# Performance work log

Measured on AMD Instinct MI355X. Metric: run time of the kernel, lower is better.

The kernel has to match this reference:

```python
import jax, jax.numpy as jnp
import numpy as np

EPS = 1e-5

def _fake_quant(w, axis):
    # symmetric int8 fake-quant with straight-through estimator
    s = jnp.max(jnp.abs(w), axis=axis, keepdims=True) / 127.0 + 1e-8
    q = jnp.clip(jnp.round(w / s), -127.0, 127.0) * s
    return w + jax.lax.stop_gradient(q - w)

def _qconv1x1(x, w, b):
    # x: [B, C_in, Q, H, W]; w: [C_out, C_in] (1x1 kernel); weight fake-quantized
    wq = _fake_quant(w, axis=1)
    return jnp.einsum('bcqhw,oc->boqhw', x, wq) + b[None, :, None, None, None]

def setup_inputs() -> dict:
    key = jax.random.key(0)
    ks = jax.random.split(key, 12)
    B, C, Q, H, W = 8, 256, 4, 40, 40
    x = jax.random.normal(ks[0], (B, C, Q, H, W), dtype=jnp.float32)
    scale = 1.0 / np.sqrt(C)
    Wq = jax.random.normal(ks[1], (C, C), dtype=jnp.float32) * scale
    Wk = jax.random.normal(ks[2], (C, C), dtype=jnp.float32) * scale
    Wv = jax.random.normal(ks[3], (C, C), dtype=jnp.float32) * scale
    Wp = jax.random.normal(ks[4], (C, C), dtype=jnp.float32) * scale
    bq = jnp.zeros((C,), jnp.float32)
    bk = jnp.zeros((C,), jnp.float32)
    bv = jnp.zeros((C,), jnp.float32)
    bp = jnp.zeros((C,), jnp.float32)
    gamma = jnp.ones((C,), jnp.float32)
    beta = jnp.zeros((C,), jnp.float32)
    return {"x": x, "Wq": Wq, "bq": bq, "Wk": Wk, "bk": bk,
            "Wv": Wv, "bv": bv, "Wp": Wp, "bp": bp,
            "gamma": gamma, "beta": beta}

def reference(x, Wq, bq, Wk, bk, Wv, bv, Wp, bp, gamma, beta):
    B, C, Q, H, W = x.shape
    q = _qconv1x1(x, Wq, bq)
    k = _qconv1x1(x, Wk, bk)
    v = _qconv1x1(x, Wv, bv)
    # per-rotation channel attention: [B, Q=4, C, H*W]
    qh = q.reshape(B, C, Q, H * W).transpose(0, 2, 1, 3)
    kh = k.reshape(B, C, Q, H * W).transpose(0, 2, 1, 3)
    vh = v.reshape(B, C, Q, H * W).transpose(0, 2, 1, 3)
    scale = 1.0 / jnp.sqrt(jnp.float32(C // 4))
    attn = jnp.einsum('bqcn,bqdn->bqcd', qh, kh) * scale  # [B,4,C,C]
    attn = jax.nn.softmax(attn, axis=-1)
    out = jnp.einsum('bqcd,bqdn->bqcn', attn, vh)  # [B,4,C,HW]
    out = out.transpose(0, 2, 1, 3).reshape(B, C, Q, H, W)
    out = _qconv1x1(out, Wp, bp)
    # IQBN: per-channel batchnorm with int8 fake-quantized gamma
    mean = jnp.mean(out, axis=(0, 2, 3, 4), keepdims=True)
    var = jnp.var(out, axis=(0, 2, 3, 4), keepdims=True)
    g = _fake_quant(gamma, axis=None)[None, :, None, None, None]
    b = beta[None, :, None, None, None]
    out = (out - mean) * jax.lax.rsqrt(var + EPS) * g + b
    return out
```

## Files before the change

### kernel.cpp

```cpp
#include <hip/hip_runtime.h>
#include <math.h>

#define BB 8
#define CCH 256
#define QQ 4
#define NN 1600
#define BQN 32
#define SP 51200
#define EPSF 1e-5f

typedef __attribute__((ext_vector_type(8))) short bf16x8;
typedef __attribute__((ext_vector_type(4))) float f32x4;

static __device__ inline ushort f2bf(float f) {
  union { float f; unsigned u; } v; v.f = f;
  return (ushort)((v.u + 0x7fffu + ((v.u >> 16) & 1u)) >> 16);
}
static __device__ inline float bf2f(ushort u) {
  union { unsigned u; float f; } v; v.u = ((unsigned)u) << 16;
  return v.f;
}
static __device__ inline void gld16(const ushort* g, ushort* l) {
  __builtin_amdgcn_global_load_lds(
      (const __attribute__((address_space(1))) unsigned int*)g,
      (__attribute__((address_space(3))) unsigned int*)l, 16, 0, 0);
}

__global__ __launch_bounds__(256)
void qp_kernel(const float* __restrict__ Wq, const float* __restrict__ Wk,
               const float* __restrict__ Wv, const float* __restrict__ Wp,
               const float* __restrict__ gamma, const float* __restrict__ x,
               ushort* __restrict__ wq, ushort* __restrict__ wk,
               ushort* __restrict__ wvT, ushort* __restrict__ wp,
               ushort* __restrict__ wqT, ushort* __restrict__ wkT,
               ushort* __restrict__ wpT, float* __restrict__ gq,
               ushort* __restrict__ xb, ushort* __restrict__ xT,
               float* __restrict__ rpart) {
  __shared__ float red[256];
  __shared__ ushort lT[64 * 66];
  int blk = blockIdx.x;
  int tid = threadIdx.x;
  if (blk < 1024) {
    int mat = blk >> 8;
    int row = blk & 255;
    const float* W = (mat == 0) ? Wq : (mat == 1) ? Wk : (mat == 2) ? Wv : Wp;
    float w = W[row * 256 + tid];
    red[tid] = fabsf(w);
    __syncthreads();
    for (int s = 128; s > 0; s >>= 1) {
      if (tid < s) red[tid] = fmaxf(red[tid], red[tid + s]);
      __syncthreads();
    }
    float s = red[0] / 127.0f + 1e-8f;
    float q = fminf(fmaxf(rintf(w / s), -127.0f), 127.0f) * s;
    ushort qb = f2bf(q);
    if (mat == 0)      { wq[row * 256 + tid] = qb; wqT[tid * 256 + row] = qb; }
    else if (mat == 1) { wk[row * 256 + tid] = qb; wkT[tid * 256 + row] = qb; }
    else if (mat == 2) { wvT[tid * 256 + row] = qb; }
    else               { wp[row * 256 + tid] = qb; wpT[tid * 256 + row] = qb; }
    return;
  }
  if (blk == 1024) {
    float g = gamma[tid];
    red[tid] = fabsf(g);
    __syncthreads();
    for (int s = 128; s > 0; s >>= 1) {
      if (tid < s) red[tid] = fmaxf(red[tid], red[tid + s]);
      __syncthreads();
    }
    float s = red[0] / 127.0f + 1e-8f;
    gq[tid] = fminf(fmaxf(rintf(g / s), -127.0f), 127.0f) * s;
    return;
  }
  int p = blk - 1025;
  int sx = p % 25;
  int rem = p / 25;
  int cy = rem & 3, bqi = rem >> 2;
  int b = bqi >> 2, q = bqi & 3;
  int s0 = sx * 64, c0 = cy * 64;
  int c = tid >> 2, nch = (tid & 3) * 16;
  const float* xp = x + ((size_t)(b * CCH + c0 + c) * QQ + q) * NN + s0 + nch;
  union { ushort u[16]; int4 v[2]; } nb;
  float s = 0.f;
#pragma unroll
  for (int j = 0; j < 4; j++) {
    float4 f = ((const float4*)xp)[j];
    ushort b0 = f2bf(f.x), b1 = f2bf(f.y), b2 = f2bf(f.z), b3 = f2bf(f.w);
    s += bf2f(b0) + bf2f(b1) + bf2f(b2) + bf2f(b3);
    nb.u[j * 4 + 0] = b0;
    nb.u[j * 4 + 1] = b1;
    nb.u[j * 4 + 2] = b2;
    nb.u[j * 4 + 3] = b3;
    lT[c * 66 + nch + j * 4 + 0] = b0;
    lT[c * 66 + nch + j * 4 + 1] = b1;
    lT[c * 66 + nch + j * 4 + 2] = b2;
    lT[c * 66 + nch + j * 4 + 3] = b3;
  }
  ushort* xbp = xb + (size_t)bqi * (CCH * NN) + (size_t)(c0 + c) * NN + s0 + nch;
  *(int4*)xbp = nb.v[0];
  *((int4*)xbp + 1) = nb.v[1];
  s += __shfl_down(s, 2);
  s += __shfl_down(s, 1);
  if ((tid & 3) == 0) rpart[((size_t)bqi * 25 + sx) * 256 + c0 + c] = s;
  __syncthreads();
  int n = tid >> 2, cch = (tid & 3) * 16;
  union { ushort u[16]; int4 v[2]; } o;
#pragma unroll
  for (int i = 0; i < 16; i++) o.u[i] = lT[(cch + i) * 66 + n];
  ushort* dst = xT + (size_t)(bqi * NN + s0 + n) * CCH + c0 + cch;
  *(int4*)dst = o.v[0];
  *((int4*)dst + 1) = o.v[1];
}

__global__ __launch_bounds__(256)
void gram_uv_kernel(const ushort* __restrict__ xb, ushort* __restrict__ Gh,
                    ushort* __restrict__ Gl,
                    const ushort* __restrict__ wqT, const ushort* __restrict__ wkT,
                    const float* __restrict__ rpart, float* __restrict__ r,
                    float* __restrict__ u, float* __restrict__ vv) {
  __shared__ __align__(16) char smem[16384];
  __shared__ float rs[256];
  int lin = blockIdx.x + 11 * blockIdx.y;
  int k8 = lin & 7, j = lin >> 3;
  int z = 4 * k8 + j / 11, t = j % 11;
  int tid = threadIdx.x;
  if (t == 10) {
    float rv = 0.f;
#pragma unroll
    for (int k = 0; k < 25; k++) rv += rpart[((size_t)z * 25 + k) * 256 + tid];
    rs[tid] = rv;
    r[z * 256 + tid] = rv;
    __syncthreads();
    float su = 0.f, sv = 0.f;
    for (int i = 0; i < 256; i++) {
      float rr = rs[i];
      su += bf2f(wqT[i * 256 + tid]) * rr;
      sv += bf2f(wkT[i * 256 + tid]) * rr;
    }
    u[z * 256 + tid] = su;
    vv[z * 256 + tid] = sv;
    return;
  }
  int ty = (t >= 4) + (t >= 7) + (t >= 9);
  int base = ty * 4 - (ty * (ty - 1)) / 2;
  int tx = ty + (t - base);
  int mBase = ty * 64, nBase = tx * 64;
  bool offd = (tx != ty);
  int wave = tid >> 6, lane = tid & 63;
  int wm = wave >> 1, wn = wave & 1;
  int col = lane & 15, quad = lane >> 4;
  const ushort* X = xb + (size_t)z * (CCH * NN);
  const ushort* gA = X + (size_t)(mBase + (tid >> 2)) * NN + (tid & 3) * 8;
  const ushort* gB = X + (size_t)(nBase + (tid >> 2)) * NN + (tid & 3) * 8;
  f32x4 acc[2][2];
#pragma unroll
  for (int i = 0; i < 2; i++)
#pragma unroll
    for (int j2 = 0; j2 < 2; j2++) acc[i][j2] = (f32x4){0.f, 0.f, 0.f, 0.f};

  const int nIter = NN / 32;
  gld16(gA, (ushort*)smem + tid * 8);
  gld16(gB, (ushort*)(smem + 4096) + tid * 8);
  for (int it = 0; it < nIter; ++it) {
    int cur = it & 1;
    __syncthreads();
    if (it + 1 < nIter) {
      int kt = (it + 1) << 5;
      char* bb = smem + (cur ^ 1) * 8192;
      gld16(gA + kt, (ushort*)bb + tid * 8);
      gld16(gB + kt, (ushort*)(bb + 4096) + tid * 8);
    }
    const ushort* lA = (const ushort*)(smem + cur * 8192);
    const ushort* lB = lA + 2048;
    bf16x8 af[2], bfr[2];
#pragma unroll
    for (int i = 0; i < 2; i++)
      af[i] = *(const bf16x8*)&lA[(wm * 32 + i * 16 + col) * 32 + quad * 8];
#pragma unroll
    for (int j2 = 0; j2 < 2; j2++)
      bfr[j2] = *(const bf16x8*)&lB[(wn * 32 + j2 * 16 + col) * 32 + quad * 8];
#pragma unroll
    for (int i = 0; i < 2; i++)
#pragma unroll
      for (int j2 = 0; j2 < 2; j2++)
        acc[i][j2] = __builtin_amdgcn_mfma_f32_16x16x32_bf16(af[i], bfr[j2], acc[i][j2], 0, 0, 0);
  }
  __syncthreads();
  float* lCw = (float*)smem + wave * 576;
#pragma unroll
  for (int i = 0; i < 2; i++) {
#pragma unroll
    for (int j2 = 0; j2 < 2; j2++)
#pragma unroll
      for (int rg = 0; rg < 4; rg++)
        lCw[(quad * 4 + rg) * 36 + j2 * 16 + col] = acc[i][j2][rg];
    int mrow0 = mBase + wm * 32 + i * 16;
    int nW = nBase + wn * 32;
    int rr = lane >> 2, cc = (lane & 3) * 8;
    union { ushort u[8]; int4 v; } oh, ol;
#pragma unroll
    for (int t8 = 0; t8 < 8; t8++) {
      float vfl = lCw[rr * 36 + cc + t8];
      ushort hh = f2bf(vfl);
      oh.u[t8] = hh;
      ol.u[t8] = f2bf(vfl - bf2f(hh));
    }
    size_t off = (size_t)z * 65536 + (size_t)(mrow0 + rr) * 256 + nW + cc;
    *(int4*)(Gh + off) = oh.v;
    *(int4*)(Gl + off) = ol.v;
    if (offd) {
      int nn = lane >> 1, mh = (lane & 1) * 8;
      union { ushort u[8]; int4 v; } th, tl;
#pragma unroll
      for (int t8 = 0; t8 < 8; t8++) {
        float vfl = lCw[(mh + t8) * 36 + nn];
        ushort hh = f2bf(vfl);
        th.u[t8] = hh;
        tl.u[t8] = f2bf(vfl - bf2f(hh));
      }
      size_t offT = (size_t)z * 65536 + (size_t)(nW + nn) * 256 + mrow0 + mh;
      *(int4*)(Gh + offT) = th.v;
      *(int4*)(Gl + offT) = tl.v;
    }
  }
}

__global__ __launch_bounds__(256)
void spk_kernel(const ushort* __restrict__ wq, const ushort* __restrict__ Gh,
                const ushort* __restrict__ Gl, const ushort* __restrict__ wk,
                const float* __restrict__ ug, const float* __restrict__ vg,
                const float* __restrict__ bqv, const float* __restrict__ bkv,
                const float* __restrict__ bvv,
                ushort* __restrict__ P, float* __restrict__ pb) {
  __shared__ __align__(16) char smem[103424];
  int lin = blockIdx.x + 8 * blockIdx.y;
  int k8 = lin & 7, j9 = lin >> 3;
  int z = 4 * k8 + (j9 >> 3), mBase = (j9 & 7) * 32;
  int tid = threadIdx.x, wave = tid >> 6, lane = tid & 63;
  int col = lane & 15, quad = lane >> 4;
  int rA = tid >> 2, sub = (tid & 3) * 8;
  const ushort* Ghz = Gh + (size_t)z * 65536;
  const ushort* Glz = Gl + (size_t)z * 65536;
  ushort* M1h_l = (ushort*)(smem + 69632);
  ushort* M1l_l = M1h_l + 8448;

  f32x4 acc[2][4];
#pragma unroll
  for (int i = 0; i < 2; i++)
#pragma unroll
    for (int j = 0; j < 4; j++) acc[i][j] = (f32x4){0.f, 0.f, 0.f, 0.f};

  auto s1_load = [&](int buf, int kt) {
    ushort* L = (ushort*)(smem + buf * 34816);
    if (tid < 128)
      gld16(wq + (size_t)(mBase + rA) * 256 + kt + sub, L + tid * 8);
    ushort* Lh = L + 1024;
    ushort* Ll = L + 9216;
#pragma unroll
    for (int q = 0; q < 4; q++) {
      int n = q * 64 + rA;
      gld16(Ghz + (size_t)n * 256 + kt + sub, Lh + (q * 256 + tid) * 8);
      gld16(Glz + (size_t)n * 256 + kt + sub, Ll + (q * 256 + tid) * 8);
    }
  };
  s1_load(0, 0);
  for (int it = 0; it < 8; ++it) {
    int cur = it & 1;
    __syncthreads();
    if (it + 1 < 8) s1_load(cur ^ 1, (it + 1) * 32);
    const ushort* L = (const ushort*)(smem + cur * 34816);
    const ushort* lA = L;
    const ushort* lBh = L + 1024;
    const ushort* lBl = L + 9216;
    bf16x8 af[2], bh[4], bl[4];
#pragma unroll
    for (int i = 0; i < 2; i++)
      af[i] = *(const bf16x8*)&lA[(i * 16 + col) * 32 + quad * 8];
#pragma unroll
    for (int j = 0; j < 4; j++) {
      bh[j] = *(const bf16x8*)&lBh[(wave * 64 + j * 16 + col) * 32 + quad * 8];
      bl[j] = *(const bf16x8*)&lBl[(wave * 64 + j * 16 + col) * 32 + quad * 8];
    }
#pragma unroll
    for (int i = 0; i < 2; i++)
#pragma unroll
      for (int j = 0; j < 4; j++) {
        acc[i][j] = __builtin_amdgcn_mfma_f32_16x16x32_bf16(af[i], bh[j], acc[i][j], 0, 0, 0);
        acc[i][j] = __builtin_amdgcn_mfma_f32_16x16x32_bf16(af[i], bl[j], acc[i][j], 0, 0, 0);
      }
  }
#pragma unroll
  for (int i = 0; i < 2; i++)
#pragma unroll
    for (int j = 0; j < 4; j++)
#pragma unroll
      for (int rg = 0; rg < 4; rg++) {
        int ml = i * 16 + quad * 4 + rg;
        int cg = wave * 64 + j * 16 + col;
        float vfl = acc[i][j][rg];
        ushort hh = f2bf(vfl);
        M1h_l[ml * 264 + cg] = hh;
        M1l_l[ml * 264 + cg] = f2bf(vfl - bf2f(hh));
      }

  f32x4 acc2[2][4];
#pragma unroll
  for (int i = 0; i < 2; i++)
#pragma unroll
    for (int j = 0; j < 4; j++) acc2[i][j] = (f32x4){0.f, 0.f, 0.f, 0.f};
  auto s2_load = [&](int buf, int kt) {
    ushort* L = (ushort*)(smem + buf * 34816);
#pragma unroll
    for (int q = 0; q < 4; q++)
      gld16(wk + (size_t)(q * 64 + rA) * 256 + kt + sub, L + (q * 256 + tid) * 8);
  };
  s2_load(0, 0);
  for (int it = 0; it < 8; ++it) {
    int cur = it & 1;
    __syncthreads();
    if (it + 1 < 8) s2_load(cur ^ 1, (it + 1) * 32);
    const ushort* lB = (const ushort*)(smem + cur * 34816);
    int kt = it * 32;
    bf16x8 ah[2], al[2], bfr[4];
#pragma unroll
    for (int i = 0; i < 2; i++) {
      ah[i] = *(const bf16x8*)&M1h_l[(i * 16 + col) * 264 + kt + quad * 8];
      al[i] = *(const bf16x8*)&M1l_l[(i * 16 + col) * 264 + kt + quad * 8];
    }
#pragma unroll
    for (int j = 0; j < 4; j++)
      bfr[j] = *(const bf16x8*)&lB[(wave * 64 + j * 16 + col) * 32 + quad * 8];
#pragma unroll
    for (int i = 0; i < 2; i++)
#pragma unroll
      for (int j = 0; j < 4; j++) {
        acc2[i][j] = __builtin_amdgcn_mfma_f32_16x16x32_bf16(ah[i], bfr[j], acc2[i][j], 0, 0, 0);
        acc2[i][j] = __builtin_amdgcn_mfma_f32_16x16x32_bf16(al[i], bfr[j], acc2[i][j], 0, 0, 0);
      }
  }
  __syncthreads();

  float* Sb = (float*)(smem + 69632);
  float bkc[4], vvc[4];
#pragma unroll
  for (int j = 0; j < 4; j++) {
    int cg = wave * 64 + j * 16 + col;
    bkc[j] = bkv[cg];
    vvc[j] = vg[z * 256 + cg];
  }
#pragma unroll
  for (int i = 0; i < 2; i++)
#pragma unroll
    for (int rg = 0; rg < 4; rg++) {
      int ml = i * 16 + quad * 4 + rg;
      int rglob = mBase + ml;
      float uu = ug[z * 256 + rglob];
      float bqc = bqv[rglob];
#pragma unroll
      for (int j = 0; j < 4; j++)
        Sb[ml * 260 + wave * 64 + j * 16 + col] =
            0.125f * (acc2[i][j][rg] + uu * bkc[j] + bqc * vvc[j] + 1600.0f * bqc * bkc[j]);
    }
  __syncthreads();

  float4 bv4 = *(const float4*)(bvv + lane * 4);
#pragma unroll
  for (int rr8 = 0; rr8 < 8; ++rr8) {
    int rloc = wave * 8 + rr8;
    f32x4 sv = *(const f32x4*)&Sb[rloc * 260 + lane * 4];
    float x0 = sv[0], x1 = sv[1], x2 = sv[2], x3 = sv[3];
    float m = fmaxf(fmaxf(x0, x1), fmaxf(x2, x3));
#pragma unroll
    for (int s = 32; s > 0; s >>= 1) m = fmaxf(m, __shfl_xor(m, s));
    float e0 = expf(x0 - m), e1 = expf(x1 - m), e2 = expf(x2 - m), e3 = expf(x3 - m);
    float t = e0 + e1 + e2 + e3;
#pragma unroll
    for (int s = 32; s > 0; s >>= 1) t += __shfl_xor(t, s);
    float is = 1.0f / t;
    float p0 = e0 * is, p1 = e1 * is, p2 = e2 * is, p3 = e3 * is;
    union { ushort u[4]; uint2 v; } o;
    o.u[0] = f2bf(p0); o.u[1] = f2bf(p1); o.u[2] = f2bf(p2); o.u[3] = f2bf(p3);
    *(uint2*)(P + (size_t)z * 65536 + (size_t)(mBase + rloc) * 256 + lane * 4) = o.v;
    float d = p0 * bv4.x + p1 * bv4.y + p2 * bv4.z + p3 * bv4.w;
#pragma unroll
    for (int s = 32; s > 0; s >>= 1) d += __shfl_xor(d, s);
    if (lane == 0) pb[z * 256 + mBase + rloc] = d;
  }
}

__global__ __launch_bounds__(256)
void pt_kernel(const ushort* __restrict__ P, const ushort* __restrict__ wvT,
               const ushort* __restrict__ wp,
               ushort* __restrict__ Tm, ushort* __restrict__ TmT,
               float* __restrict__ m_acc, float* __restrict__ v_acc) {
  __shared__ __align__(16) char smem[53760];
  int lin = blockIdx.x + 8 * blockIdx.y;
  int k8 = lin & 7, j9 = lin >> 3;
  int z = 4 * k8 + (j9 >> 3), cs = (j9 & 7) * 32;
  int tid = threadIdx.x, wave = tid >> 6, lane = tid & 63;
  int col = lane & 15, quad = lane >> 4;
  int rA = tid >> 2, sub = (tid & 3) * 8;
  if (lin == 0) {
    m_acc[tid] = 0.f;
    v_acc[tid] = 0.f;
  }
  const ushort* Pz = P + (size_t)z * 65536;
  ushort* N1b = (ushort*)(smem + 36864);

  f32x4 acc[4][2];
#pragma unroll
  for (int i = 0; i < 4; i++)
#pragma unroll
    for (int j = 0; j < 2; j++) acc[i][j] = (f32x4){0.f, 0.f, 0.f, 0.f};
  auto s3_load = [&](int buf, int kt) {
    ushort* L = (ushort*)(smem + buf * 18432);
#pragma unroll
    for (int q = 0; q < 4; q++)
      gld16(Pz + (size_t)(q * 64 + rA) * 256 + kt + sub, L + (q * 256 + tid) * 8);
    if (tid < 128)
      gld16(wvT + (size_t)(cs + rA) * 256 + kt + sub, L + 8192 + tid * 8);
  };
  s3_load(0, 0);
  for (int it = 0; it < 8; ++it) {
    int cur = it & 1;
    __syncthreads();
    if (it + 1 < 8) s3_load(cur ^ 1, (it + 1) * 32);
    const ushort* lP = (const ushort*)(smem + cur * 18432);
    const ushort* lV = lP + 8192;
    bf16x8 af[4], bfr[2];
#pragma unroll
    for (int i = 0; i < 4; i++)
      af[i] = *(const bf16x8*)&lP[(wave * 64 + i * 16 + col) * 32 + quad * 8];
#pragma unroll
    for (int j = 0; j < 2; j++)
      bfr[j] = *(const bf16x8*)&lV[(j * 16 + col) * 32 + quad * 8];
#pragma unroll
    for (int i = 0; i < 4; i++)
#pragma unroll
      for (int j = 0; j < 2; j++)
        acc[i][j] = __builtin_amdgcn_mfma_f32_16x16x32_bf16(af[i], bfr[j], acc[i][j], 0, 0, 0);
  }
#pragma unroll
  for (int i = 0; i < 4; i++)
#pragma unroll
    for (int j = 0; j < 2; j++)
#pragma unroll
      for (int rg = 0; rg < 4; rg++) {
        int e = wave * 64 + i * 16 + quad * 4 + rg;
        int cl = j * 16 + col;
        N1b[cl * 264 + e] = f2bf(acc[i][j][rg]);
      }

  f32x4 acc2[4][2];
#pragma unroll
  for (int i = 0; i < 4; i++)
#pragma unroll
    for (int j = 0; j < 2; j++) acc2[i][j] = (f32x4){0.f, 0.f, 0.f, 0.f};
  auto s4_load = [&](int buf, int kt) {
    ushort* L = (ushort*)(smem + buf * 18432);
#pragma unroll
    for (int q = 0; q < 4; q++)
      gld16(wp + (size_t)(q * 64 + rA) * 256 + kt + sub, L + (q * 256 + tid) * 8);
  };
  s4_load(0, 0);
  for (int it = 0; it < 8; ++it) {
    int cur = it & 1;
    __syncthreads();
    if (it + 1 < 8) s4_load(cur ^ 1, (it + 1) * 32);
    const ushort* lW = (const ushort*)(smem + cur * 18432);
    int kt = it * 32;
    bf16x8 af[4], bfr[2];
#pragma unroll
    for (int i = 0; i < 4; i++)
      af[i] = *(const bf16x8*)&lW[(wave * 64 + i * 16 + col) * 32 + quad * 8];
#pragma unroll
    for (int j = 0; j < 2; j++)
      bfr[j] = *(const bf16x8*)&N1b[(j * 16 + col) * 264 + kt + quad * 8];
#pragma unroll
    for (int i = 0; i < 4; i++)
#pragma unroll
      for (int j = 0; j < 2; j++)
        acc2[i][j] = __builtin_amdgcn_mfma_f32_16x16x32_bf16(af[i], bfr[j], acc2[i][j], 0, 0, 0);
  }
  __syncthreads();
  float* lCw = (float*)smem + wave * 576;
#pragma unroll
  for (int i = 0; i < 4; i++) {
#pragma unroll
    for (int j = 0; j < 2; j++)
#pragma unroll
      for (int rg = 0; rg < 4; rg++)
        lCw[(quad * 4 + rg) * 36 + j * 16 + col] = acc2[i][j][rg];
    int oW = wave * 64 + i * 16;
    int rr = lane >> 2, cc = (lane & 3) * 8;
    union { ushort u[8]; int4 v; } o;
#pragma unroll
    for (int t8 = 0; t8 < 8; t8++) o.u[t8] = f2bf(lCw[rr * 36 + cc + t8]);
    *(int4*)(Tm + (size_t)z * 65536 + (size_t)(oW + rr) * 256 + cs + cc) = o.v;
    int nn = lane >> 1, mh = (lane & 1) * 8;
    union { ushort u[8]; int4 v; } o2;
#pragma unroll
    for (int t8 = 0; t8 < 8; t8++) o2.u[t8] = f2bf(lCw[(mh + t8) * 36 + nn]);
    *(int4*)(TmT + (size_t)z * 65536 + (size_t)(cs + nn) * 256 + oW + mh) = o2.v;
  }
}

__global__ __launch_bounds__(256)
void dsq_bo_kernel(const ushort* __restrict__ Tm, const ushort* __restrict__ Gh,
                   const ushort* __restrict__ Gl,
                   const ushort* __restrict__ wpT, const ushort* __restrict__ TmT,
                   const float* __restrict__ pb, const float* __restrict__ rb,
                   const float* __restrict__ bp, float* __restrict__ bo,
                   float* __restrict__ m_acc, float* __restrict__ v_acc) {
  __shared__ __align__(16) char smem[24576];
  int blk = blockIdx.x;
  int tid = threadIdx.x;
  if (blk >= 512) {
    int z = blk - 512;
    float* sp = (float*)smem;
    float* sr = sp + 256;
    sp[tid] = pb[z * 256 + tid];
    sr[tid] = rb[z * 256 + tid];
    __syncthreads();
    float bv = bp[tid], d1 = 0.f;
    const ushort* Tz = TmT + (size_t)z * 65536;
    for (int c = 0; c < 256; c++) {
      bv += bf2f(wpT[c * 256 + tid]) * sp[c];
      d1 += bf2f(Tz[c * 256 + tid]) * sr[c];
    }
    bo[z * 256 + tid] = bv;
    atomicAdd(m_acc + tid, d1 + 1600.0f * bv);
    atomicAdd(v_acc + tid, 2.0f * bv * d1 + 1600.0f * bv * bv);
    return;
  }
  int k8 = blk & 7, j9 = blk >> 3;
  int z = 4 * k8 + (j9 >> 4);
  int tile = j9 & 15;
  int mBase = (tile >> 2) * 64, nBase = (tile & 3) * 64;
  int wave = tid >> 6, lane = tid & 63;
  int wm = wave >> 1, wn = wave & 1;
  int col = lane & 15, quad = lane >> 4;
  int srow = tid >> 2, skc = (tid & 3) * 8;
  const ushort* Tz = Tm + (size_t)z * 65536;
  const ushort* gA = Tz + (size_t)(mBase + srow) * 256 + skc;
  const ushort* gB = Gh + (size_t)z * 65536 + (size_t)(nBase + srow) * 256 + skc;
  const ushort* gX = Gl + (size_t)z * 65536 + (size_t)(nBase + srow) * 256 + skc;

  f32x4 acc[2][2];
#pragma unroll
  for (int i = 0; i < 2; i++)
#pragma unroll
    for (int j = 0; j < 2; j++) acc[i][j] = (f32x4){0.f, 0.f, 0.f, 0.f};

  {
    char* bb = smem;
    gld16(gA, (ushort*)bb + tid * 8);
    gld16(gB, (ushort*)(bb + 4096) + tid * 8);
    gld16(gX, (ushort*)(bb + 8192) + tid * 8);
  }
  for (int it = 0; it < 8; ++it) {
    int cur = it & 1;
    __syncthreads();
    if (it + 1 < 8) {
      int kt = (it + 1) * 32;
      char* bb = smem + (cur ^ 1) * 12288;
      gld16(gA + kt, (ushort*)bb + tid * 8);
      gld16(gB + kt, (ushort*)(bb + 4096) + tid * 8);
      gld16(gX + kt, (ushort*)(bb + 8192) + tid * 8);
    }
    const ushort* lA = (const ushort*)(smem + cur * 12288);
    const ushort* lB = lA + 2048;
    const ushort* lX = lA + 4096;
    bf16x8 af[2], bfv[2], xf[2];
#pragma unroll
    for (int i = 0; i < 2; i++)
      af[i] = *(const bf16x8*)&lA[(wm * 32 + i * 16 + col) * 32 + quad * 8];
#pragma unroll
    for (int j = 0; j < 2; j++) {
      bfv[j] = *(const bf16x8*)&lB[(wn * 32 + j * 16 + col) * 32 + quad * 8];
      xf[j]  = *(const bf16x8*)&lX[(wn * 32 + j * 16 + col) * 32 + quad * 8];
    }
#pragma unroll
    for (int i = 0; i < 2; i++)
#pragma unroll
      for (int j = 0; j < 2; j++) {
        acc[i][j] = __builtin_amdgcn_mfma_f32_16x16x32_bf16(af[i], bfv[j], acc[i][j], 0, 0, 0);
        acc[i][j] = __builtin_amdgcn_mfma_f32_16x16x32_bf16(af[i], xf[j], acc[i][j], 0, 0, 0);
      }
  }
#pragma unroll
  for (int i = 0; i < 2; i++) {
    int mr = mBase + wm * 32 + i * 16 + quad * 4;
#pragma unroll
    for (int rg = 0; rg < 4; rg++) {
      float p = 0.f;
#pragma unroll
      for (int j = 0; j < 2; j++)
        p += acc[i][j][rg] * bf2f(Tz[(mr + rg) * 256 + nBase + wn * 32 + j * 16 + col]);
      p += __shfl_down(p, 8);
      p += __shfl_down(p, 4);
      p += __shfl_down(p, 2);
      p += __shfl_down(p, 1);
      if (col == 0) atomicAdd(v_acc + mr + rg, p);
    }
  }
}

__global__ __launch_bounds__(256)
void final_kernel(const ushort* __restrict__ Tm, const ushort* __restrict__ xT,
                  const float* __restrict__ bo, const float* __restrict__ m_acc,
                  const float* __restrict__ v_acc, const float* __restrict__ gq,
                  const float* __restrict__ beta, float* __restrict__ out) {
  __shared__ __align__(16) char smem[32768];
  float* lC = (float*)smem;
  int lin = blockIdx.x + 13 * blockIdx.y + 26 * blockIdx.z;
  int k8 = lin % 8, j9 = lin / 8;
  int z = 4 * k8 + j9 / 26;
  int tile = j9 % 26;
  int mBase = (tile / 13) * 128, nBase = (tile % 13) * 128;
  int tid = threadIdx.x, wave = tid >> 6, lane = tid & 63;
  int wm = wave >> 1, wn = wave & 1;
  int col = lane & 15, quad = lane >> 4;
  int srow = tid >> 2, skc = (tid & 3) * 8;
  const ushort* Az = Tm + (size_t)z * 65536;
  const ushort* Bz = xT + (size_t)z * (NN * 256);
  const ushort* gA  = Az + (size_t)(mBase + srow) * 256 + skc;
  const ushort* gA2 = gA + 64 * 256;
  int br1 = nBase + srow;      br1 = br1 < NN ? br1 : NN - 1;
  int br2 = nBase + 64 + srow; br2 = br2 < NN ? br2 : NN - 1;
  const ushort* gB  = Bz + (size_t)br1 * 256 + skc;
  const ushort* gB2 = Bz + (size_t)br2 * 256 + skc;
  ushort* sA1[2]; ushort* sA2[2]; ushort* sB1[2]; ushort* sB2[2];
#pragma unroll
  for (int b = 0; b < 2; b++) {
    ushort* lAb = (ushort*)(smem + b * 16384);
    ushort* lBb = (ushort*)(smem + b * 16384 + 8192);
    sA1[b] = &lAb[srow * 32 + skc];
    sA2[b] = &lAb[(64 + srow) * 32 + skc];
    sB1[b] = &lBb[srow * 32 + skc];
    sB2[b] = &lBb[(64 + srow) * 32 + skc];
  }
  f32x4 acc[4][4];
#pragma unroll
  for (int i = 0; i < 4; i++)
#pragma unroll
    for (int j = 0; j < 4; j++) acc[i][j] = (f32x4){0.f, 0.f, 0.f, 0.f};

  const int nIter = 8;
  gld16(gA, sA1[0]); gld16(gA2, sA2[0]); gld16(gB, sB1[0]); gld16(gB2, sB2[0]);
  for (int it = 0; it < nIter; ++it) {
    int cur = it & 1;
    __syncthreads();
    if (it + 1 < nIter) {
      int kt = (it + 1) << 5, nxt = cur ^ 1;
      gld16(gA + kt, sA1[nxt]); gld16(gA2 + kt, sA2[nxt]);
      gld16(gB + kt, sB1[nxt]); gld16(gB2 + kt, sB2[nxt]);
    }
    const ushort* lAc = (const ushort*)(smem + cur * 16384);
    const ushort* lBc = (const ushort*)(smem + cur * 16384 + 8192);
    bf16x8 af[4], bfr[4];
#pragma unroll
    for (int i = 0; i < 4; i++)
      af[i] = *(const bf16x8*)&lAc[(wm * 64 + i * 16 + col) * 32 + quad * 8];
#pragma unroll
    for (int j = 0; j < 4; j++)
      bfr[j] = *(const bf16x8*)&lBc[(wn * 64 + j * 16 + col) * 32 + quad * 8];
#pragma unroll
    for (int i = 0; i < 4; i++)
#pragma unroll
      for (int j = 0; j < 4; j++)
        acc[i][j] = __builtin_amdgcn_mfma_f32_16x16x32_bf16(af[i], bfr[j], acc[i][j], 0, 0, 0);
  }
  __syncthreads();
  float* lCw = lC + wave * 16 * 68;
  int mW = mBase + wm * 64, nW = nBase + wn * 64;
  int b = z >> 2, q = z & 3;
  const float inv = 1.0f / (float)SP;
#pragma unroll
  for (int i = 0; i < 4; i++) {
#pragma unroll
    for (int j = 0; j < 4; j++)
#pragma unroll
      for (int rg = 0; rg < 4; rg++)
        lCw[(quad * 4 + rg) * 68 + j * 16 + col] = acc[i][j][rg];
    int mrow0 = mW + i * 16;
    int rr = lane & 15, cc = lane >> 4;
    int n0 = nW + cc * 16;
    int o = mrow0 + rr;
    float bi = bo[(size_t)z * 256 + o];
    float mean = m_acc[o] * inv;
    float var = v_acc[o] * inv - mean * mean;
    float scl = rsqrtf(var + EPSF) * gq[o];
    float be = beta[o];
    if (n0 < NN) {
      float* C = out + (size_t)b * (CCH * QQ * NN)
               + (size_t)o * (QQ * NN) + (size_t)q * NN + n0;
#pragma unroll
      for (int v = 0; v < 4; v++) {
        float4 f;
        f.x = (lCw[rr * 68 + cc * 16 + v * 4 + 0] + bi - mean) * scl + be;
        f.y = (lCw[rr * 68 + cc * 16 + v * 4 + 1] + bi - mean) * scl + be;
        f.z = (lCw[rr * 68 + cc * 16 + v * 4 + 2] + bi - mean) * scl + be;
        f.w = (lCw[rr * 68 + cc * 16 + v * 4 + 3] + bi - mean) * scl + be;
        *(float4*)(C + v * 4) = f;
      }
    }
  }
}

extern "C" void kernel_launch(void* const* d_in, const int* in_sizes, int n_in,
                              void* d_out, int out_size, void* d_ws, size_t ws_size,
                              hipStream_t stream) {
  const float* x     = (const float*)d_in[0];
  const float* Wq    = (const float*)d_in[1];
  const float* bq    = (const float*)d_in[2];
  const float* Wk    = (const float*)d_in[3];
  const float* bk    = (const float*)d_in[4];
  const float* Wv    = (const float*)d_in[5];
  const float* bv    = (const float*)d_in[6];
  const float* Wp    = (const float*)d_in[7];
  const float* bp    = (const float*)d_in[8];
  const float* gamma = (const float*)d_in[9];
  const float* beta  = (const float*)d_in[10];
  float* out = (float*)d_out;

  ushort* h    = (ushort*)d_ws;
  ushort* wq   = h;
  ushort* wk   = wq + 65536;
  ushort* wp   = wk + 65536;
  ushort* wvT  = wp + 65536;
  ushort* wqT  = wvT + 65536;
  ushort* wkT  = wqT + 65536;
  ushort* wpT  = wkT + 65536;
  ushort* xb   = wpT + 65536;
  ushort* xT   = xb + (size_t)BQN * CCH * NN;
  ushort* Gh   = xT + (size_t)BQN * CCH * NN;
  ushort* Gl   = Gh + (size_t)BQN * 65536;
  ushort* P    = Gl + (size_t)BQN * 65536;
  ushort* Tm   = P + (size_t)BQN * 65536;
  ushort* TmT  = Tm + (size_t)BQN * 65536;
  float*  r    = (float*)(TmT + (size_t)BQN * 65536);
  float*  u    = r + 8192;
  float*  vv   = u + 8192;
  float*  pb   = vv + 8192;
  float*  bo   = pb + 8192;
  float*  m_acc = bo + 8192;
  float*  v_acc = m_acc + 256;
  float*  gq   = v_acc + 256;
  float*  rpart = gq + 256;

  qp_kernel<<<4225, 256, 0, stream>>>(Wq, Wk, Wv, Wp, gamma, x,
                                      wq, wk, wvT, wp, wqT, wkT, wpT, gq,
                                      xb, xT, rpart);
  gram_uv_kernel<<<dim3(11, BQN), 256, 0, stream>>>(xb, Gh, Gl, wqT, wkT,
                                                    rpart, r, u, vv);
  spk_kernel<<<dim3(8, BQN), 256, 0, stream>>>(wq, Gh, Gl, wk, u, vv, bq, bk, bv, P, pb);
  pt_kernel<<<dim3(8, BQN), 256, 0, stream>>>(P, wvT, wp, Tm, TmT, m_acc, v_acc);
  dsq_bo_kernel<<<544, 256, 0, stream>>>(Tm, Gh, Gl, wpT, TmT, pb, r, bp,
                                         bo, m_acc, v_acc);
  final_kernel<<<dim3(13, 2, BQN), 256, 0, stream>>>(Tm, xT, bo, m_acc, v_acc,
                                                     gq, beta, out);
}
```

Before: 239.6 us.

## Exploit Gram matrix symmetry in variance quadratic form with K-split tiles

The variance term computes a quadratic form T·G·Tᵀ row-wise, and G is symmetric. The kernel now takes only the upper-triangular 64x64 blocks of G (10 of 16), doubles the off-diagonal contributions, and gives each block its own 64-wide K slice, so each block loads everything once and runs no K loop. This roughly halves the MFMA work and raises the block count from 512 to 1280 for more parallelism. The cost is more atomics into v_acc and a reliance on G being exactly symmetric (Gh/Gl splits).

```diff
diff --git a/kernel.cpp b/kernel.cpp
--- a/kernel.cpp
+++ b/kernel.cpp
@@ -515,8 +515,8 @@
   __shared__ __align__(16) char smem[24576];
   int blk = blockIdx.x;
   int tid = threadIdx.x;
-  if (blk >= 512) {
-    int z = blk - 512;
+  if (blk >= 1280) {
+    int z = blk - 1280;
     float* sp = (float*)smem;
     float* sr = sp + 256;
     sp[tid] = pb[z * 256 + tid];
@@ -534,58 +534,57 @@
     return;
   }
   int k8 = blk & 7, j9 = blk >> 3;
-  int z = 4 * k8 + (j9 >> 4);
-  int tile = j9 & 15;
-  int mBase = (tile >> 2) * 64, nBase = (tile & 3) * 64;
+  int z = 4 * k8 + j9 / 40;
+  int rem = j9 % 40;
+  int mt = rem / 10, t = rem % 10;
+  int ty = (t >= 4) + (t >= 7) + (t >= 9);
+  int base = ty * 4 - (ty * (ty - 1)) / 2;
+  int tx = ty + (t - base);
+  int mBase = mt * 64, aBase = ty * 64, bBase = tx * 64;
+  float mul = (tx == ty) ? 1.0f : 2.0f;
   int wave = tid >> 6, lane = tid & 63;
   int wm = wave >> 1, wn = wave & 1;
   int col = lane & 15, quad = lane >> 4;
   int srow = tid >> 2, skc = (tid & 3) * 8;
   const ushort* Tz = Tm + (size_t)z * 65536;
-  const ushort* gA = Tz + (size_t)(mBase + srow) * 256 + skc;
-  const ushort* gB = Gh + (size_t)z * 65536 + (size_t)(nBase + srow) * 256 + skc;
-  const ushort* gX = Gl + (size_t)z * 65536 + (size_t)(nBase + srow) * 256 + skc;
-
+  const ushort* Ghz = Gh + (size_t)z * 65536;
+  const ushort* Glz = Gl + (size_t)z * 65536;
+  ushort* lA = (ushort*)smem;
+  ushort* lH = lA + 4096;
+  ushort* lL = lH + 4096;
+#pragma unroll
+  for (int c = 0; c < 2; c++) {
+    int ko = aBase + c * 32 + skc;
+    gld16(Tz + (size_t)(mBase + srow) * 256 + ko, lA + c * 2048 + tid * 8);
+    gld16(Ghz + (size_t)(bBase + srow) * 256 + ko, lH + c * 2048 + tid * 8);
+    gld16(Glz + (size_t)(bBase + srow) * 256 + ko, lL + c * 2048 + tid * 8);
+  }
   f32x4 acc[2][2];
 #pragma unroll
   for (int i = 0; i < 2; i++)
 #pragma unroll
     for (int j = 0; j < 2; j++) acc[i][j] = (f32x4){0.f, 0.f, 0.f, 0.f};
-
-  {
-    char* bb = smem;
-    gld16(gA, (ushort*)bb + tid * 8);
-    gld16(gB, (ushort*)(bb + 4096) + tid * 8);
-    gld16(gX, (ushort*)(bb + 8192) + tid * 8);
-  }
-  for (int it = 0; it < 8; ++it) {
-    int cur = it & 1;
-    __syncthreads();
-    if (it + 1 < 8) {
-      int kt = (it + 1) * 32;
-      char* bb = smem + (cur ^ 1) * 12288;
-      gld16(gA + kt, (ushort*)bb + tid * 8);
-      gld16(gB + kt, (ushort*)(bb + 4096) + tid * 8);
-      gld16(gX + kt, (ushort*)(bb + 8192) + tid * 8);
-    }
-    const ushort* lA = (const ushort*)(smem + cur * 12288);
-    const ushort* lB = lA + 2048;
-    const ushort* lX = lA + 4096;
-    bf16x8 af[2], bfv[2], xf[2];
+  __syncthreads();
+#pragma unroll
+  for (int c = 0; c < 2; c++) {
+    const ushort* cA = lA + c * 2048;
+    const ushort* cH = lH + c * 2048;
+    const ushort* cL = lL + c * 2048;
+    bf16x8 af[2], bh[2], bl[2];
 #pragma unroll
     for (int i = 0; i < 2; i++)
-      af[i] = *(const bf16x8*)&lA[(wm * 32 + i * 16 + col) * 32 + quad * 8];
+      af[i] = *(const bf16x8*)&cA[(wm * 32 + i * 16 + col) * 32 + quad * 8];
 #pragma unroll
     for (int j = 0; j < 2; j++) {
-      bfv[j] = *(const bf16x8*)&lB[(wn * 32 + j * 16 + col) * 32 + quad * 8];
-      xf[j]  = *(const bf16x8*)&lX[(wn * 32 + j * 16 + col) * 32 + quad * 8];
+      bh[j] = *(const bf16x8*)&cH[(wn * 32 + j * 16 + col) * 32 + quad * 8];
+      bl[j] = *(const bf16x8*)&cL[(wn * 32 + j * 16 + col) * 32 + quad * 8];
     }
 #pragma unroll
     for (int i = 0; i < 2; i++)
 #pragma unroll
       for (int j = 0; j < 2; j++) {
-        acc[i][j] = __builtin_amdgcn_mfma_f32_16x16x32_bf16(af[i], bfv[j], acc[i][j], 0, 0, 0);
-        acc[i][j] = __builtin_amdgcn_mfma_f32_16x16x32_bf16(af[i], xf[j], acc[i][j], 0, 0, 0);
+        acc[i][j] = __builtin_amdgcn_mfma_f32_16x16x32_bf16(af[i], bh[j], acc[i][j], 0, 0, 0);
+        acc[i][j] = __builtin_amdgcn_mfma_f32_16x16x32_bf16(af[i], bl[j], acc[i][j], 0, 0, 0);
       }
   }
 #pragma unroll
@@ -596,12 +595,12 @@
       float p = 0.f;
 #pragma unroll
       for (int j = 0; j < 2; j++)
-        p += acc[i][j][rg] * bf2f(Tz[(mr + rg) * 256 + nBase + wn * 32 + j * 16 + col]);
+        p += acc[i][j][rg] * bf2f(Tz[(mr + rg) * 256 + bBase + wn * 32 + j * 16 + col]);
       p += __shfl_down(p, 8);
       p += __shfl_down(p, 4);
       p += __shfl_down(p, 2);
       p += __shfl_down(p, 1);
-      if (col == 0) atomicAdd(v_acc + mr + rg, p);
+      if (col == 0) atomicAdd(v_acc + mr + rg, p * mul);
     }
   }
 }
@@ -756,8 +755,8 @@
                                                     rpart, r, u, vv);
   spk_kernel<<<dim3(8, BQN), 256, 0, stream>>>(wq, Gh, Gl, wk, u, vv, bq, bk, bv, P, pb);
   pt_kernel<<<dim3(8, BQN), 256, 0, stream>>>(P, wvT, wp, Tm, TmT, m_acc, v_acc);
-  dsq_bo_kernel<<<544, 256, 0, stream>>>(Tm, Gh, Gl, wpT, TmT, pb, r, bp,
-                                         bo, m_acc, v_acc);
+  dsq_bo_kernel<<<1312, 256, 0, stream>>>(Tm, Gh, Gl, wpT, TmT, pb, r, bp,
+                                          bo, m_acc, v_acc);
   final_kernel<<<dim3(13, 2, BQN), 256, 0, stream>>>(Tm, xT, bo, m_acc, v_acc,
                                                      gq, beta, out);
 }
```

Result: slower. 275.3 us (+14.9%).
